# Optimization experiments

Hardware: AMD Instinct MI355X
Metric: run time of the kernel (lower is better)

## Reference

```python
import jax, jax.numpy as jnp
import numpy as np

N = 8192  # number of proposals


def setup_inputs() -> dict:
    key = jax.random.key(0)
    k1, k2, k3 = jax.random.split(key, 3)
    xy = jax.random.uniform(k1, (N, 2), dtype=jnp.float32) * 1000.0   # top-left corners
    wh = jax.random.uniform(k2, (N, 2), dtype=jnp.float32) * 120.0 + 4.0  # widths/heights
    conf = jax.random.uniform(k3, (N, 1), dtype=jnp.float32)
    preds = jnp.concatenate([xy, xy + wh, conf], axis=1)  # [N,5] x1,y1,x2,y2,conf
    return {"preds": preds, "thresh": 0.5, "max_proposals": 1000}


def _nms_keep_mask(boxes_sorted, thresh):
    # boxes_sorted: [N,4] sorted by descending confidence
    x1, y1, x2, y2 = (boxes_sorted[:, i] for i in range(4))
    area = (x2 - x1) * (y2 - y1)                               # [N]
    ix1 = jnp.maximum(x1[:, None], x1[None, :])
    iy1 = jnp.maximum(y1[:, None], y1[None, :])
    ix2 = jnp.minimum(x2[:, None], x2[None, :])
    iy2 = jnp.minimum(y2[:, None], y2[None, :])
    iw = jnp.maximum(ix2 - ix1, 0.0)
    ih = jnp.maximum(iy2 - iy1, 0.0)
    inter = iw * ih                                            # [N,N]
    iou = inter / (area[:, None] + area[None, :] - inter + 1e-12)
    n = boxes_sorted.shape[0]
    later = jnp.arange(n)[None, :] > jnp.arange(n)[:, None]    # strictly lower-priority boxes

    def body(i, keep):
        # if box i survives, suppress all later boxes overlapping it above thresh
        sup = keep[i] & later[i] & (iou[i] > thresh)
        return keep & ~sup

    return jax.lax.fori_loop(0, n, body, jnp.ones((n,), dtype=bool))


def reference(preds, thresh, max_proposals):
    # thresh < 0 -> identity (original early return); implemented with thresh >= 0 path
    order = jnp.argsort(-preds[:, 4])          # descending confidence
    boxes_sorted = preds[order, :4]
    keep = _nms_keep_mask(boxes_sorted, thresh)  # [N] bool, in sorted order
    n = preds.shape[0]
    # stable pack: kept positions first (ascending = descending confidence), pad at end
    rank = jnp.where(keep, jnp.arange(n), n)
    pos = jnp.argsort(rank)[:max_proposals]     # [M] positions in sorted order
    valid = keep[pos]                           # [M] which slots are real
    keep_idx = jnp.where(valid, order[pos], -1)  # indices into original preds, -1 pad
    kept = preds[jnp.clip(keep_idx, 0)]          # [M,5]
    kept = jnp.where(valid[:, None], kept, 0.0)
    return kept, keep_idx
```

## Files before the change

### kernel.cpp

```cpp
#include <hip/hip_runtime.h>

typedef unsigned long long u64;

#define FSLOTS 16
#define RCUT 2048

__global__ __launch_bounds__(256)
void k_rank_part(const float* __restrict__ preds, int n, int cpb,
                 int* __restrict__ pc) {
  __shared__ float cs[1024];
  int c0 = blockIdx.y * cpb;
  int cn = min(cpb, n - c0);
  for (int j = threadIdx.x; j < cn; j += blockDim.x)
    cs[j] = preds[(c0 + j) * 5 + 4];
  __syncthreads();
  int i = blockIdx.x * blockDim.x + threadIdx.x;
  if (i >= n) return;
  float ci = preds[i * 5 + 4];
  int cnt = 0;
  const float4* cs4 = (const float4*)cs;
  int cn4 = cn >> 2;
  for (int j4 = 0; j4 < cn4; ++j4) {
    float4 c4 = cs4[j4];
    int jb = c0 + j4 * 4;
    cnt += (c4.x > ci) || (c4.x == ci && (jb + 0) < i);
    cnt += (c4.y > ci) || (c4.y == ci && (jb + 1) < i);
    cnt += (c4.z > ci) || (c4.z == ci && (jb + 2) < i);
    cnt += (c4.w > ci) || (c4.w == ci && (jb + 3) < i);
  }
  for (int j = cn4 * 4; j < cn; ++j)
    cnt += (cs[j] > ci) || (cs[j] == ci && (c0 + j) < i);
  pc[(size_t)blockIdx.y * n + i] = cnt;
}

__global__ __launch_bounds__(256)
void k_scatter(const float* __restrict__ preds, const int* __restrict__ pc,
               int n, int nyb, float* __restrict__ sboxes,
               int* __restrict__ sidx, int* __restrict__ rowcnt) {
  int i = blockIdx.x * blockDim.x + threadIdx.x;
  if (i >= n) return;
  rowcnt[i] = 0;
  int pos = 0;
  for (int y = 0; y < nyb; ++y) pos += pc[(size_t)y * n + i];
  sboxes[pos * 4 + 0] = preds[i * 5 + 0];
  sboxes[pos * 4 + 1] = preds[i * 5 + 1];
  sboxes[pos * 4 + 2] = preds[i * 5 + 2];
  sboxes[pos * 4 + 3] = preds[i * 5 + 3];
  sidx[pos] = i;
}

__global__ void k_mask(const float* __restrict__ sboxes, int n,
                       const float* __restrict__ thr_p,
                       u64* __restrict__ M, u64* __restrict__ D1,
                       int* __restrict__ rowcnt, int* __restrict__ rowlist,
                       int nw, int Rw, int mode, const int* __restrict__ done) {
  int wx = blockIdx.x;
  int ry = blockIdx.y;
  if (wx < ry) return;
  if (mode == 1) {
    if (wx < Rw && ry < Rw) return;
    if (*done) return;
  }
  int lane = threadIdx.x;

  __shared__ float4 cb[64];
  __shared__ float cbar[64];
  const float4* sb4 = (const float4*)sboxes;
  int col0 = wx * 64;
  int cj = col0 + lane;
  int cjc = cj < n ? cj : n - 1;
  {
    float4 b4 = sb4[cjc];
    cb[lane] = b4;
    cbar[lane] = __fmul_rn(__fsub_rn(b4.z, b4.x), __fsub_rn(b4.w, b4.y));
  }
  __syncthreads();

  int row = ry * 64 + lane;
  if (row >= n) return;
  float th = *thr_p;
  float4 r4 = sb4[row];
  float rarea = __fmul_rn(__fsub_rn(r4.z, r4.x), __fsub_rn(r4.w, r4.y));

  u64 w = 0;
#pragma unroll 8
  for (int j = 0; j < 64; ++j) {
    float4 c4 = cb[j];
    float ix1 = fmaxf(r4.x, c4.x);
    float iy1 = fmaxf(r4.y, c4.y);
    float ix2 = fminf(r4.z, c4.z);
    float iy2 = fminf(r4.w, c4.w);
    float iw = fmaxf(__fsub_rn(ix2, ix1), 0.0f);
    float ih = fmaxf(__fsub_rn(iy2, iy1), 0.0f);
    float inter = __fmul_rn(iw, ih);
    float denom = __fadd_rn(__fsub_rn(__fadd_rn(rarea, cbar[j]), inter), 1e-12f);
    float iou = __fdiv_rn(inter, denom);
    int col = col0 + j;
    bool sup = (col > row) && (col < n) && (iou > th);
    w |= ((u64)sup) << j;
  }
  M[(size_t)row * nw + wx] = w;
  if (wx == ry) D1[row] = w;
  u64 w2 = w;
  while (w2) {
    int j = (int)__builtin_ctzll(w2);
    w2 &= w2 - 1;
    int idx = atomicAdd(&rowcnt[row], 1);
    if (idx < FSLOTS) rowlist[(size_t)row * FSLOTS + idx] = col0 + j;
  }
}

__device__ __forceinline__ u64 bcast64(u64 v, int b) {
  unsigned lo = __builtin_amdgcn_readlane((unsigned)v, b);
  unsigned hi = __builtin_amdgcn_readlane((unsigned)(v >> 32), b);
  return ((u64)hi << 32) | lo;
}

__device__ __forceinline__ u64 sgpr64(u64 v) {
  unsigned lo = __builtin_amdgcn_readfirstlane((unsigned)v);
  unsigned hi = __builtin_amdgcn_readfirstlane((unsigned)(v >> 32));
  return ((u64)hi << 32) | lo;
}

__device__ __forceinline__ u64 wor64(u64 v) {
#pragma unroll
  for (int off = 32; off; off >>= 1)
    v |= __shfl_xor(v, off, 64);
  return v;
}

#define APPLYJ(JV, T)                                                      \
  if ((T) < lim_) {                                                        \
    int j_ = (JV);                                                         \
    atomicAnd(&live[j_ >> 6], ~((u64)1 << (j_ & 63)));                     \
  }

#define CHUNK(c, BND, RC, LA, LB, LC, LD)                                  \
  if (out < maxp && (c) < nch) {                                           \
    u64 rem_ = sgpr64(live[(c)]);                                          \
    if (rem_) {                                                            \
      u64 K_;                                                              \
      u64 my_ = ((rem_ >> lane) & 1) ? (BND) : 0;                          \
      u64 A_ = sgpr64(wor64(my_));                                         \
      u64 hot_ = rem_ & A_;                                                \
      if (!hot_) {                                                         \
        K_ = rem_;                                                         \
      } else {                                                             \
        u64 defK_ = rem_ & ~A_;                                            \
        u64 myk_ = ((defK_ >> lane) & 1) ? (BND) : 0;                      \
        u64 S_ = sgpr64(wor64(myk_));                                      \
        K_ = defK_;                                                        \
        while (hot_) {                                                     \
          int b_ = __builtin_amdgcn_readfirstlane(                         \
              (int)__builtin_ctzll(hot_));                                 \
          hot_ &= hot_ - 1;                                                \
          if (!((S_ >> b_) & 1)) {                                         \
            K_ |= (u64)1 << b_;                                            \
            S_ |= bcast64(BND, b_);                                        \
          }                                                                \
        }                                                                  \
      }                                                                    \
      int kc_ = (int)__popcll(K_);                                         \
      bool mine_ = (K_ >> lane) & 1;                                       \
      if (mine_) {                                                         \
        int pos_ = out + (int)__popcll(K_ & (((u64)1 << lane) - 1));       \
        if (pos_ < maxp) sel[pos_] = (c) * 64 + lane;                      \
      }                                                                    \
      out += kc_;                                                          \
      if (kc_ > 0 && out < maxp) {                                         \
        int lim_ = mine_ ? ((RC) < FSLOTS ? (RC) : FSLOTS) : 0;            \
        APPLYJ((LA).x, 0)  APPLYJ((LA).y, 1)                               \
        APPLYJ((LA).z, 2)  APPLYJ((LA).w, 3)                               \
        APPLYJ((LB).x, 4)  APPLYJ((LB).y, 5)                               \
        APPLYJ((LB).z, 6)  APPLYJ((LB).w, 7)                               \
        APPLYJ((LC).x, 8)  APPLYJ((LC).y, 9)                               \
        APPLYJ((LC).z, 10) APPLYJ((LC).w, 11)                              \
        APPLYJ((LD).x, 12) APPLYJ((LD).y, 13)                              \
        APPLYJ((LD).z, 14) APPLYJ((LD).w, 15)                              \
        u64 ovf_ = __ballot(mine_ && (RC) > FSLOTS);                       \
        while (ovf_) {                                                     \
          int l_ = (int)__builtin_ctzll(ovf_);                             \
          ovf_ &= ovf_ - 1;                                                \
          int r_ = (c) * 64 + l_;                                          \
          u64 v0_ = (2 * lane < nch)                                       \
                        ? M[(size_t)r_ * nw + 2 * lane] : 0ULL;            \
          u64 v1_ = (2 * lane + 1 < nch)                                   \
                        ? M[(size_t)r_ * nw + 2 * lane + 1] : 0ULL;        \
          live[2 * lane] &= ~v0_;                                          \
          live[2 * lane + 1] &= ~v1_;                                      \
        }                                                                  \
      }                                                                    \
    }                                                                      \
    {                                                                      \
      int cc_ = (c) + 4;                                                   \
      if (cc_ < nch) {                                                     \
        int r_ = cc_ * 64 + lane;                                          \
        int rr_ = r_ < n ? r_ : n - 1;                                     \
        BND = D1[rr_];                                                     \
        RC = rowcnt[rr_];                                                  \
        const int4* lp_ = (const int4*)(rowlist + (size_t)rr_ * FSLOTS);   \
        LA = lp_[0]; LB = lp_[1]; LC = lp_[2]; LD = lp_[3];                \
      }                                                                    \
    }                                                                      \
  }

#define PREF(cc, BND, RC, LA, LB, LC, LD)                                  \
  if ((cc) < nch) {                                                        \
    int r_ = (cc) * 64 + lane;                                             \
    int rr_ = r_ < n ? r_ : n - 1;                                         \
    BND = D1[rr_];                                                         \
    RC = rowcnt[rr_];                                                      \
    const int4* lp_ = (const int4*)(rowlist + (size_t)rr_ * FSLOTS);       \
    LA = lp_[0]; LB = lp_[1]; LC = lp_[2]; LD = lp_[3];                    \
  }

__global__ __launch_bounds__(64, 1)
void k_scan(const u64* __restrict__ M, const u64* __restrict__ D1,
            const int* __restrict__ rowcnt, const int* __restrict__ rowlist,
            int n, int nw, int maxp, int nch_lim, int mode,
            int* __restrict__ done,
            int* __restrict__ sel, int* __restrict__ cnt) {
  if (mode == 1 && *done) return;
  __shared__ u64 live[128];
  int lane = threadIdx.x;
  int nch = nch_lim;

  for (int w = lane; w < 128; w += 64) {
    u64 m = 0;
    if (w < nw) {
      long long hi = (long long)(w + 1) * 64;
      m = (hi <= n) ? ~0ULL
                    : ((n > (long long)w * 64)
                           ? (((u64)1 << (n - w * 64)) - 1) : 0ULL);
    }
    live[w] = m;
  }

  u64 b0 = 0, b1 = 0, b2 = 0, b3 = 0;
  int rc0 = 0, rc1 = 0, rc2 = 0, rc3 = 0;
  int4 l00 = {0,0,0,0}, l01 = {0,0,0,0}, l02 = {0,0,0,0}, l03 = {0,0,0,0};
  int4 l10 = {0,0,0,0}, l11 = {0,0,0,0}, l12 = {0,0,0,0}, l13 = {0,0,0,0};
  int4 l20 = {0,0,0,0}, l21 = {0,0,0,0}, l22 = {0,0,0,0}, l23 = {0,0,0,0};
  int4 l30 = {0,0,0,0}, l31 = {0,0,0,0}, l32 = {0,0,0,0}, l33 = {0,0,0,0};
  PREF(0, b0, rc0, l00, l01, l02, l03)
  PREF(1, b1, rc1, l10, l11, l12, l13)
  PREF(2, b2, rc2, l20, l21, l22, l23)
  PREF(3, b3, rc3, l30, l31, l32, l33)

  int out = 0;

  for (int kk = 0; kk < nch && out < maxp; kk += 4) {
    CHUNK(kk + 0, b0, rc0, l00, l01, l02, l03)
    CHUNK(kk + 1, b1, rc1, l10, l11, l12, l13)
    CHUNK(kk + 2, b2, rc2, l20, l21, l22, l23)
    CHUNK(kk + 3, b3, rc3, l30, l31, l32, l33)
  }
  if (lane == 0) {
    *cnt = (out < maxp) ? out : maxp;
    if (mode == 0) *done = (out >= maxp || nch_lim >= nw) ? 1 : 0;
  }
}

__global__ void k_emit(const float* __restrict__ preds,
                       const int* __restrict__ sidx,
                       const int* __restrict__ sel,
                       const int* __restrict__ cnt,
                       int maxp, float* __restrict__ out) {
  int k = blockIdx.x * blockDim.x + threadIdx.x;
  if (k >= maxp) return;
  int nk = *cnt;
  if (k < nk) {
    int p = sel[k];
    int orig = sidx[p];
#pragma unroll
    for (int q = 0; q < 5; ++q) out[k * 5 + q] = preds[orig * 5 + q];
    out[(size_t)maxp * 5 + k] = (float)orig;
  } else {
#pragma unroll
    for (int q = 0; q < 5; ++q) out[k * 5 + q] = 0.0f;
    out[(size_t)maxp * 5 + k] = -1.0f;
  }
}

extern "C" void kernel_launch(void* const* d_in, const int* in_sizes, int n_in,
                              void* d_out, int out_size, void* d_ws, size_t ws_size,
                              hipStream_t stream) {
  const float* preds = (const float*)d_in[0];
  const float* thr   = (const float*)d_in[1];
  float* out = (float*)d_out;
  int n    = in_sizes[0] / 5;
  int maxp = out_size / 6;
  int nw   = (n + 63) / 64;
  int Rw   = (RCUT / 64 < nw) ? RCUT / 64 : nw;
  int cpb  = 1024;
  int nyb  = (n + cpb - 1) / cpb;

  char* ws = (char*)d_ws;
  u64* M = (u64*)ws;
  size_t off = (size_t)n * nw * sizeof(u64);
  u64* D1 = (u64*)(ws + off);  off += (size_t)n * sizeof(u64);
  float* sboxes = (float*)(ws + off);  off += (size_t)n * 4 * sizeof(float);
  int*   sidx   = (int*)(ws + off);    off += (size_t)n * sizeof(int);
  int*   sel    = (int*)(ws + off);    off += (size_t)maxp * sizeof(int);
  int*   cnt    = (int*)(ws + off);    off += sizeof(int) * 4;
  int*   done   = (int*)(ws + off);    off += sizeof(int) * 4;
  int*   rowcnt = (int*)(ws + off);    off += (size_t)n * sizeof(int);
  int*   rowlist= (int*)(ws + off);    off += (size_t)n * FSLOTS * sizeof(int);
  int*   pc     = (int*)(ws + off);

  hipLaunchKernelGGL(k_rank_part, dim3((n + 255) / 256, nyb), dim3(256), 0,
                     stream, preds, n, cpb, pc);
  hipLaunchKernelGGL(k_scatter, dim3((n + 255) / 256), dim3(256), 0, stream,
                     preds, pc, n, nyb, sboxes, sidx, rowcnt);
  hipLaunchKernelGGL(k_mask, dim3(Rw, Rw), dim3(64), 0, stream,
                     sboxes, n, thr, M, D1, rowcnt, rowlist, nw, Rw, 0, done);
  hipLaunchKernelGGL(k_scan, dim3(1), dim3(64), 0, stream,
                     M, D1, rowcnt, rowlist, n, nw, maxp, Rw, 0, done, sel, cnt);
  hipLaunchKernelGGL(k_mask, dim3(nw, nw), dim3(64), 0, stream,
                     sboxes, n, thr, M, D1, rowcnt, rowlist, nw, Rw, 1, done);
  hipLaunchKernelGGL(k_scan, dim3(1), dim3(64), 0, stream,
                     M, D1, rowcnt, rowlist, n, nw, maxp, nw, 1, done, sel, cnt);
  hipLaunchKernelGGL(k_emit, dim3((maxp + 255) / 256), dim3(256), 0, stream,
                     preds, sidx, sel, cnt, maxp, out);
}
```

Measured before the change: 75.61 us.

## Fuse fallback scan with emit, compact triangular mask grid, batch rowlist atomics

The fallback mask launch now enumerates only the needed upper-triangle tiles outside the first Rw×Rw block, using a 1D grid with a triangular index decode. Blocks that previously launched only to exit immediately are no longer created. The second scan and the emit kernel are merged into one k_finish kernel, removing a launch. The per-bit atomicAdd on rowcnt is replaced by one atomicAdd of the popcount, which cuts atomic traffic in the mask kernel.

```diff
diff --git a/kernel.cpp b/kernel.cpp
--- a/kernel.cpp
+++ b/kernel.cpp
@@ -54,12 +54,17 @@
                        u64* __restrict__ M, u64* __restrict__ D1,
                        int* __restrict__ rowcnt, int* __restrict__ rowlist,
                        int nw, int Rw, int mode, const int* __restrict__ done) {
-  int wx = blockIdx.x;
-  int ry = blockIdx.y;
-  if (wx < ry) return;
-  if (mode == 1) {
-    if (wx < Rw && ry < Rw) return;
+  int wx, ry;
+  if (mode == 0) {
+    wx = blockIdx.x; ry = blockIdx.y;
+    if (wx < ry) return;
+  } else {
     if (*done) return;
+    int u = blockIdx.x + (Rw * (Rw + 1)) / 2;
+    int w = (int)((sqrt(8.0 * u + 1.0) - 1.0) * 0.5);
+    while ((w + 1) * (w + 2) / 2 <= u) ++w;
+    while (w * (w + 1) / 2 > u) --w;
+    wx = w; ry = u - w * (w + 1) / 2;
   }
   int lane = threadIdx.x;
 
@@ -101,12 +106,18 @@
   }
   M[(size_t)row * nw + wx] = w;
   if (wx == ry) D1[row] = w;
-  u64 w2 = w;
-  while (w2) {
-    int j = (int)__builtin_ctzll(w2);
-    w2 &= w2 - 1;
-    int idx = atomicAdd(&rowcnt[row], 1);
-    if (idx < FSLOTS) rowlist[(size_t)row * FSLOTS + idx] = col0 + j;
+  int pcw = (int)__popcll(w);
+  if (pcw) {
+    int base = atomicAdd(&rowcnt[row], pcw);
+    u64 w2 = w;
+    int k = 0;
+    while (w2) {
+      int j = (int)__builtin_ctzll(w2);
+      w2 &= w2 - 1;
+      int idx = base + k;
+      if (idx < FSLOTS) rowlist[(size_t)row * FSLOTS + idx] = col0 + j;
+      ++k;
+    }
   }
 }
 
@@ -214,71 +225,89 @@
     LA = lp_[0]; LB = lp_[1]; LC = lp_[2]; LD = lp_[3];                    \
   }
 
+#define SCAN_BODY(NCH_)                                                    \
+  int nch = (NCH_);                                                        \
+  for (int w = lane; w < 128; w += 64) {                                   \
+    u64 m = 0;                                                             \
+    if (w < nw) {                                                          \
+      long long hi = (long long)(w + 1) * 64;                              \
+      m = (hi <= n) ? ~0ULL                                                \
+                    : ((n > (long long)w * 64)                             \
+                           ? (((u64)1 << (n - w * 64)) - 1) : 0ULL);       \
+    }                                                                      \
+    live[w] = m;                                                           \
+  }                                                                        \
+  u64 b0 = 0, b1 = 0, b2 = 0, b3 = 0;                                      \
+  int rc0 = 0, rc1 = 0, rc2 = 0, rc3 = 0;                                  \
+  int4 l00 = {0,0,0,0}, l01 = {0,0,0,0}, l02 = {0,0,0,0}, l03 = {0,0,0,0}; \
+  int4 l10 = {0,0,0,0}, l11 = {0,0,0,0}, l12 = {0,0,0,0}, l13 = {0,0,0,0}; \
+  int4 l20 = {0,0,0,0}, l21 = {0,0,0,0}, l22 = {0,0,0,0}, l23 = {0,0,0,0}; \
+  int4 l30 = {0,0,0,0}, l31 = {0,0,0,0}, l32 = {0,0,0,0}, l33 = {0,0,0,0}; \
+  PREF(0, b0, rc0, l00, l01, l02, l03)                                     \
+  PREF(1, b1, rc1, l10, l11, l12, l13)                                     \
+  PREF(2, b2, rc2, l20, l21, l22, l23)                                     \
+  PREF(3, b3, rc3, l30, l31, l32, l33)                                     \
+  int out = 0;                                                             \
+  for (int kk = 0; kk < nch && out < maxp; kk += 4) {                      \
+    CHUNK(kk + 0, b0, rc0, l00, l01, l02, l03)                             \
+    CHUNK(kk + 1, b1, rc1, l10, l11, l12, l13)                             \
+    CHUNK(kk + 2, b2, rc2, l20, l21, l22, l23)                             \
+    CHUNK(kk + 3, b3, rc3, l30, l31, l32, l33)                             \
+  }
+
 __global__ __launch_bounds__(64, 1)
-void k_scan(const u64* __restrict__ M, const u64* __restrict__ D1,
-            const int* __restrict__ rowcnt, const int* __restrict__ rowlist,
-            int n, int nw, int maxp, int nch_lim, int mode,
-            int* __restrict__ done,
-            int* __restrict__ sel, int* __restrict__ cnt) {
-  if (mode == 1 && *done) return;
+void k_scan_try(const u64* __restrict__ M, const u64* __restrict__ D1,
+                const int* __restrict__ rowcnt, const int* __restrict__ rowlist,
+                int n, int nw, int maxp, int nch_lim,
+                int* __restrict__ done,
+                int* __restrict__ sel, int* __restrict__ cnt) {
   __shared__ u64 live[128];
   int lane = threadIdx.x;
-  int nch = nch_lim;
-
-  for (int w = lane; w < 128; w += 64) {
-    u64 m = 0;
-    if (w < nw) {
-      long long hi = (long long)(w + 1) * 64;
-      m = (hi <= n) ? ~0ULL
-                    : ((n > (long long)w * 64)
-                           ? (((u64)1 << (n - w * 64)) - 1) : 0ULL);
-    }
-    live[w] = m;
-  }
-
-  u64 b0 = 0, b1 = 0, b2 = 0, b3 = 0;
-  int rc0 = 0, rc1 = 0, rc2 = 0, rc3 = 0;
-  int4 l00 = {0,0,0,0}, l01 = {0,0,0,0}, l02 = {0,0,0,0}, l03 = {0,0,0,0};
-  int4 l10 = {0,0,0,0}, l11 = {0,0,0,0}, l12 = {0,0,0,0}, l13 = {0,0,0,0};
-  int4 l20 = {0,0,0,0}, l21 = {0,0,0,0}, l22 = {0,0,0,0}, l23 = {0,0,0,0};
-  int4 l30 = {0,0,0,0}, l31 = {0,0,0,0}, l32 = {0,0,0,0}, l33 = {0,0,0,0};
-  PREF(0, b0, rc0, l00, l01, l02, l03)
-  PREF(1, b1, rc1, l10, l11, l12, l13)
-  PREF(2, b2, rc2, l20, l21, l22, l23)
-  PREF(3, b3, rc3, l30, l31, l32, l33)
-
-  int out = 0;
-
-  for (int kk = 0; kk < nch && out < maxp; kk += 4) {
-    CHUNK(kk + 0, b0, rc0, l00, l01, l02, l03)
-    CHUNK(kk + 1, b1, rc1, l10, l11, l12, l13)
-    CHUNK(kk + 2, b2, rc2, l20, l21, l22, l23)
-    CHUNK(kk + 3, b3, rc3, l30, l31, l32, l33)
-  }
+  SCAN_BODY(nch_lim)
   if (lane == 0) {
     *cnt = (out < maxp) ? out : maxp;
-    if (mode == 0) *done = (out >= maxp || nch_lim >= nw) ? 1 : 0;
-  }
-}
-
-__global__ void k_emit(const float* __restrict__ preds,
-                       const int* __restrict__ sidx,
-                       const int* __restrict__ sel,
-                       const int* __restrict__ cnt,
-                       int maxp, float* __restrict__ out) {
-  int k = blockIdx.x * blockDim.x + threadIdx.x;
-  if (k >= maxp) return;
-  int nk = *cnt;
-  if (k < nk) {
-    int p = sel[k];
-    int orig = sidx[p];
+    *done = (out >= maxp || nch_lim >= nw) ? 1 : 0;
+  }
+}
+
+__global__ __launch_bounds__(256, 1)
+void k_finish(const u64* __restrict__ M, const u64* __restrict__ D1,
+              const int* __restrict__ rowcnt, const int* __restrict__ rowlist,
+              const float* __restrict__ preds, const int* __restrict__ sidx,
+              int n, int nw, int maxp, const int* __restrict__ done,
+              int* __restrict__ sel, int* __restrict__ cnt,
+              float* __restrict__ outp) {
+  __shared__ u64 live[128];
+  __shared__ int nk_s;
+  int t = threadIdx.x;
+  int dn = *done;
+  if (!dn) {
+    if (t < 64) {
+      int lane = t;
+      SCAN_BODY(nw)
+      if (lane == 0) {
+        int nk = (out < maxp) ? out : maxp;
+        *cnt = nk;
+        nk_s = nk;
+      }
+    }
+  } else {
+    if (t == 0) nk_s = *cnt;
+  }
+  __syncthreads();
+  int nk = nk_s;
+  for (int k = t; k < maxp; k += 256) {
+    if (k < nk) {
+      int p = sel[k];
+      int orig = sidx[p];
 #pragma unroll
-    for (int q = 0; q < 5; ++q) out[k * 5 + q] = preds[orig * 5 + q];
-    out[(size_t)maxp * 5 + k] = (float)orig;
-  } else {
+      for (int q = 0; q < 5; ++q) outp[k * 5 + q] = preds[orig * 5 + q];
+      outp[(size_t)maxp * 5 + k] = (float)orig;
+    } else {
 #pragma unroll
-    for (int q = 0; q < 5; ++q) out[k * 5 + q] = 0.0f;
-    out[(size_t)maxp * 5 + k] = -1.0f;
+      for (int q = 0; q < 5; ++q) outp[k * 5 + q] = 0.0f;
+      outp[(size_t)maxp * 5 + k] = -1.0f;
+    }
   }
 }
 
@@ -294,6 +323,7 @@
   int Rw   = (RCUT / 64 < nw) ? RCUT / 64 : nw;
   int cpb  = 1024;
   int nyb  = (n + cpb - 1) / cpb;
+  int hiT  = (nw * (nw + 1)) / 2 - (Rw * (Rw + 1)) / 2;
 
   char* ws = (char*)d_ws;
   u64* M = (u64*)ws;
@@ -314,12 +344,12 @@
                      preds, pc, n, nyb, sboxes, sidx, rowcnt);
   hipLaunchKernelGGL(k_mask, dim3(Rw, Rw), dim3(64), 0, stream,
                      sboxes, n, thr, M, D1, rowcnt, rowlist, nw, Rw, 0, done);
-  hipLaunchKernelGGL(k_scan, dim3(1), dim3(64), 0, stream,
-                     M, D1, rowcnt, rowlist, n, nw, maxp, Rw, 0, done, sel, cnt);
-  hipLaunchKernelGGL(k_mask, dim3(nw, nw), dim3(64), 0, stream,
-                     sboxes, n, thr, M, D1, rowcnt, rowlist, nw, Rw, 1, done);
-  hipLaunchKernelGGL(k_scan, dim3(1), dim3(64), 0, stream,
-                     M, D1, rowcnt, rowlist, n, nw, maxp, nw, 1, done, sel, cnt);
-  hipLaunchKernelGGL(k_emit, dim3((maxp + 255) / 256), dim3(256), 0, stream,
-                     preds, sidx, sel, cnt, maxp, out);
-}
+  hipLaunchKernelGGL(k_scan_try, dim3(1), dim3(64), 0, stream,
+                     M, D1, rowcnt, rowlist, n, nw, maxp, Rw, done, sel, cnt);
+  if (hiT > 0)
+    hipLaunchKernelGGL(k_mask, dim3(hiT), dim3(64), 0, stream,
+                       sboxes, n, thr, M, D1, rowcnt, rowlist, nw, Rw, 1, done);
+  hipLaunchKernelGGL(k_finish, dim3(1), dim3(256), 0, stream,
+                     M, D1, rowcnt, rowlist, preds, sidx, n, nw, maxp, done,
+                     sel, cnt, out);
+}
```

Measured after the change: 74.49 us. About the same (-1.5%).
